# Kernel optimization log

Measured on AMD Instinct MI355X. Metric: run time of the kernel, lower is better.

The kernel has to match this reference:

```python
import jax, jax.numpy as jnp
import numpy as np

N = 200000
E = 600000
H = 128
NUM_EDGE_TYPES = 16
LN_EPS = 1e-5


def setup_inputs() -> dict:
    key = jax.random.key(0)
    ks = jax.random.split(key, 10)
    x = jax.random.normal(ks[0], (N, H), dtype=jnp.float32)
    edge_index = jax.random.randint(ks[1], (2, E), 0, N, dtype=jnp.int32)
    edge_types = jax.random.randint(ks[2], (E,), 0, NUM_EDGE_TYPES, dtype=jnp.int32)
    s = 1.0 / np.sqrt(H)
    edge_emb = jax.random.normal(ks[3], (NUM_EDGE_TYPES, H), dtype=jnp.float32)
    W_self = jax.random.uniform(ks[4], (H, H), dtype=jnp.float32, minval=-s, maxval=s)
    b_self = jax.random.uniform(ks[5], (H,), dtype=jnp.float32, minval=-s, maxval=s)
    W_msg = jax.random.uniform(ks[6], (H, H), dtype=jnp.float32, minval=-s, maxval=s)
    b_msg = jax.random.uniform(ks[7], (H,), dtype=jnp.float32, minval=-s, maxval=s)
    gamma = jnp.ones((H,), dtype=jnp.float32)
    beta = jnp.zeros((H,), dtype=jnp.float32)
    return {
        "x": x, "edge_index": edge_index, "edge_types": edge_types,
        "edge_emb": edge_emb, "W_self": W_self, "b_self": b_self,
        "W_msg": W_msg, "b_msg": b_msg, "gamma": gamma, "beta": beta,
    }


def reference(x, edge_index, edge_types, edge_emb, W_self, b_self, W_msg, b_msg, gamma, beta):
    src = edge_index[0]
    dst = edge_index[1]
    # gather source node features + typed edge embedding: [E, H]
    typed_messages = x[src] + edge_emb[edge_types]
    # scatter-add into destination nodes: [N, H]
    aggregated = jnp.zeros_like(x).at[dst].add(typed_messages)
    # linear epilogue (torch Linear: y = x @ W.T + b)
    out = (x @ W_self.T + b_self) + (aggregated @ W_msg.T + b_msg)
    out = jax.nn.relu(out)
    # LayerNorm over last dim
    mu = jnp.mean(out, axis=-1, keepdims=True)
    var = jnp.mean(jnp.square(out - mu), axis=-1, keepdims=True)
    out = (out - mu) * jax.lax.rsqrt(var + LN_EPS) * gamma + beta
    # dropout is identity in eval mode
    return out
```

## Files before the change

### kernel.cpp

```cpp
#include <hip/hip_runtime.h>
#include <stdint.h>

#define H 128
#define TM 16
#define MAXDEG 24
#define BSTRIDE 32

typedef __attribute__((ext_vector_type(8))) short short8;
typedef __attribute__((ext_vector_type(4))) float f32x4;
typedef __attribute__((ext_vector_type(4))) int i32x4;

__device__ __forceinline__ unsigned short f2bf(float f) {
    union { float f; unsigned u; } v; v.f = f;
    unsigned u = v.u;
    u += 0x7fffu + ((u >> 16) & 1u);
    return (unsigned short)(u >> 16);
}

__device__ __forceinline__ float bf2f(unsigned short u) {
    union { unsigned u; float f; } v; v.u = ((unsigned)u) << 16; return v.f;
}

__device__ __forceinline__ short8 cvt8(f32x4 a, f32x4 b) {
    short8 r;
    r[0] = (short)f2bf(a.x); r[1] = (short)f2bf(a.y);
    r[2] = (short)f2bf(a.z); r[3] = (short)f2bf(a.w);
    r[4] = (short)f2bf(b.x); r[5] = (short)f2bf(b.y);
    r[6] = (short)f2bf(b.z); r[7] = (short)f2bf(b.w);
    return r;
}

__global__ __launch_bounds__(256) void prep_kernel(
    const float* __restrict__ x, const float* __restrict__ emb,
    unsigned short* __restrict__ xb, unsigned short* __restrict__ embb,
    const int* __restrict__ ei, const int* __restrict__ et,
    int* __restrict__ bucket,
    int total8x, int total8e, int E)
{
    int i = blockIdx.x * 256 + threadIdx.x;
    if (i < total8x) {
        f32x4 a = ((const f32x4*)x)[2 * i];
        f32x4 b = ((const f32x4*)x)[2 * i + 1];
        ((short8*)xb)[i] = cvt8(a, b);
    } else if (i < total8x + total8e) {
        int j = i - total8x;
        f32x4 a = ((const f32x4*)emb)[2 * j];
        f32x4 b = ((const f32x4*)emb)[2 * j + 1];
        ((short8*)embb)[j] = cvt8(a, b);
    }
    if (i < E) {
        int src = ei[i];
        int dst = ei[E + i];
        int t   = et[i];
        int* row = bucket + (size_t)dst * BSTRIDE;
        int pos = atomicAdd(row, 1);
        if (pos < MAXDEG) row[1 + pos] = src | (t << 18);
    }
}

__global__ __launch_bounds__(256) void prep_edges_kernel(
    const int* __restrict__ ei, const int* __restrict__ et,
    int* __restrict__ cnt, int* __restrict__ bucket, int E)
{
    int e = blockIdx.x * 256 + threadIdx.x;
    if (e >= E) return;
    int src = ei[e];
    int dst = ei[E + e];
    int t   = et[e];
    int pos = atomicAdd(&cnt[dst], 1);
    if (pos < MAXDEG) bucket[(size_t)dst * MAXDEG + pos] = src | (t << 18);
}

__global__ __launch_bounds__(256) void aggregate_bf16_kernel(
    const unsigned short* __restrict__ xb, const unsigned short* __restrict__ embb,
    const int* __restrict__ bucket,
    const int* __restrict__ ei, const int* __restrict__ et,
    unsigned short* __restrict__ aggb, int N, int E, int T)
{
    __shared__ __align__(16) short emb_s[16 * 136];

    const int tid = threadIdx.x;
    const int l   = tid & 15;
    if (tid < T * 16) {
        int t = tid >> 4;
        *(short8*)&emb_s[t * 136 + l * 8] = *(const short8*)(embb + t * H + l * 8);
    }
    __syncthreads();

    const int nGroups = N >> 4;
    for (int g = blockIdx.x; g < nGroups; g += gridDim.x) {
        const int node = (g << 4) + (tid >> 4);

        const int* row = bucket + (size_t)node * BSTRIDE;
        i32x4 q = *(const i32x4*)row;
        const int c = q.x;

        float acc[8] = {0.f, 0.f, 0.f, 0.f, 0.f, 0.f, 0.f, 0.f};

        if (c <= MAXDEG) {
            {
                const bool b0 = c > 0, b1 = c > 1, b2 = c > 2;
                short8 xv0, xv1, xv2, ev0, ev1, ev2;
                if (b0) {
                    int s = q.y & 0x3FFFF, t = q.y >> 18;
                    xv0 = *(const short8*)(xb + (size_t)s * H + l * 8);
                    ev0 = *(const short8*)&emb_s[t * 136 + l * 8];
                }
                if (b1) {
                    int s = q.z & 0x3FFFF, t = q.z >> 18;
                    xv1 = *(const short8*)(xb + (size_t)s * H + l * 8);
                    ev1 = *(const short8*)&emb_s[t * 136 + l * 8];
                }
                if (b2) {
                    int s = q.w & 0x3FFFF, t = q.w >> 18;
                    xv2 = *(const short8*)(xb + (size_t)s * H + l * 8);
                    ev2 = *(const short8*)&emb_s[t * 136 + l * 8];
                }
                if (b0) {
#pragma unroll
                    for (int j = 0; j < 8; ++j) acc[j] += bf2f((unsigned short)xv0[j]) + bf2f((unsigned short)ev0[j]);
                }
                if (b1) {
#pragma unroll
                    for (int j = 0; j < 8; ++j) acc[j] += bf2f((unsigned short)xv1[j]) + bf2f((unsigned short)ev1[j]);
                }
                if (b2) {
#pragma unroll
                    for (int j = 0; j < 8; ++j) acc[j] += bf2f((unsigned short)xv2[j]) + bf2f((unsigned short)ev2[j]);
                }
            }
            for (int i0 = 3; i0 < c; i0 += 4) {
                i32x4 p = *(const i32x4*)(row + 1 + i0);
                const int rem = c - i0;
                const bool h1 = rem > 1, h2 = rem > 2, h3 = rem > 3;
                short8 xv0, xv1, xv2, xv3, ev0, ev1, ev2, ev3;
                {
                    int s = p.x & 0x3FFFF, t = p.x >> 18;
                    xv0 = *(const short8*)(xb + (size_t)s * H + l * 8);
                    ev0 = *(const short8*)&emb_s[t * 136 + l * 8];
                }
                if (h1) {
                    int s = p.y & 0x3FFFF, t = p.y >> 18;
                    xv1 = *(const short8*)(xb + (size_t)s * H + l * 8);
                    ev1 = *(const short8*)&emb_s[t * 136 + l * 8];
                }
                if (h2) {
                    int s = p.z & 0x3FFFF, t = p.z >> 18;
                    xv2 = *(const short8*)(xb + (size_t)s * H + l * 8);
                    ev2 = *(const short8*)&emb_s[t * 136 + l * 8];
                }
                if (h3) {
                    int s = p.w & 0x3FFFF, t = p.w >> 18;
                    xv3 = *(const short8*)(xb + (size_t)s * H + l * 8);
                    ev3 = *(const short8*)&emb_s[t * 136 + l * 8];
                }
#pragma unroll
                for (int j = 0; j < 8; ++j) acc[j] += bf2f((unsigned short)xv0[j]) + bf2f((unsigned short)ev0[j]);
                if (h1) {
#pragma unroll
                    for (int j = 0; j < 8; ++j) acc[j] += bf2f((unsigned short)xv1[j]) + bf2f((unsigned short)ev1[j]);
                }
                if (h2) {
#pragma unroll
                    for (int j = 0; j < 8; ++j) acc[j] += bf2f((unsigned short)xv2[j]) + bf2f((unsigned short)ev2[j]);
                }
                if (h3) {
#pragma unroll
                    for (int j = 0; j < 8; ++j) acc[j] += bf2f((unsigned short)xv3[j]) + bf2f((unsigned short)ev3[j]);
                }
            }
        } else {
            for (int e = 0; e < E; ++e) {
                if (ei[E + e] == node) {
                    int s = ei[e], t = et[e];
                    short8 xv = *(const short8*)(xb + (size_t)s * H + l * 8);
                    short8 ev = *(const short8*)&emb_s[t * 136 + l * 8];
#pragma unroll
                    for (int j = 0; j < 8; ++j) acc[j] += bf2f((unsigned short)xv[j]) + bf2f((unsigned short)ev[j]);
                }
            }
        }

        short8 r;
#pragma unroll
        for (int j = 0; j < 8; ++j) r[j] = (short)f2bf(acc[j]);
        *(short8*)(aggb + (size_t)node * H + l * 8) = r;
    }
}

__global__ __launch_bounds__(256) void gemm_ln32_kernel(
    const unsigned short* __restrict__ xb, const unsigned short* __restrict__ aggb,
    const float* __restrict__ Wself, const float* __restrict__ bself,
    const float* __restrict__ Wmsg, const float* __restrict__ bmsg,
    const float* __restrict__ gamma, const float* __restrict__ beta,
    float* __restrict__ out, int nSuper)
{
    __shared__ __align__(16) short a_stage[32 * 264];
    __shared__ __align__(16) float o_stage[32 * 132];

    const int tid  = threadIdx.x;
    const int wave = tid >> 6;
    const int lane = tid & 63;
    const int col  = lane & 15;
    const int quad = lane >> 4;

    short8 bfrag[2][8];
    float bias[2];
#pragma unroll
    for (int s = 0; s < 2; ++s) {
        const int h = (wave * 2 + s) * 16 + col;
        bias[s] = bself[h] + bmsg[h];
#pragma unroll
        for (int kst = 0; kst < 8; ++kst) {
            const float* W = (kst < 4) ? Wself : Wmsg;
            const int k0 = (kst & 3) * 32 + quad * 8;
            const float* p = W + (size_t)h * H + k0;
            bfrag[s][kst] = cvt8(*(const f32x4*)p, *(const f32x4*)(p + 4));
        }
    }

    const int lrow = tid >> 4;
    const int l4 = (tid & 15) * 4;
    f32x4 g0  = *(const f32x4*)(gamma + l4);
    f32x4 g1  = *(const f32x4*)(gamma + 64 + l4);
    f32x4 be0 = *(const f32x4*)(beta + l4);
    f32x4 be1 = *(const f32x4*)(beta + 64 + l4);

    const int srow = tid >> 3;
    const int sq   = tid & 7;

    for (int st = blockIdx.x; st < nSuper; st += gridDim.x) {
        const size_t rowBase = (size_t)st * 32;

        {
            const unsigned short* src = (sq < 4)
                ? (xb   + (rowBase + srow) * H + sq * 32)
                : (aggb + (rowBase + srow) * H + (sq - 4) * 32);
            short* dstl = &a_stage[srow * 264 + (sq & 3) * 32 + ((sq >> 2) << 7)];
            *(short8*)(dstl)      = ((const short8*)src)[0];
            *(short8*)(dstl + 8)  = ((const short8*)src)[1];
            *(short8*)(dstl + 16) = ((const short8*)src)[2];
            *(short8*)(dstl + 24) = ((const short8*)src)[3];
        }
        __syncthreads();

        f32x4 acc00 = {0.f,0.f,0.f,0.f}, acc01 = {0.f,0.f,0.f,0.f};
        f32x4 acc10 = {0.f,0.f,0.f,0.f}, acc11 = {0.f,0.f,0.f,0.f};
        {
            short8 afr[8];
#pragma unroll
            for (int kst = 0; kst < 8; ++kst)
                afr[kst] = *(const short8*)&a_stage[col * 264 + kst * 32 + quad * 8];
#pragma unroll
            for (int kst = 0; kst < 8; ++kst) {
                acc00 = __builtin_amdgcn_mfma_f32_16x16x32_bf16(afr[kst], bfrag[0][kst], acc00, 0, 0, 0);
                acc01 = __builtin_amdgcn_mfma_f32_16x16x32_bf16(afr[kst], bfrag[1][kst], acc01, 0, 0, 0);
            }
#pragma unroll
            for (int kst = 0; kst < 8; ++kst)
                afr[kst] = *(const short8*)&a_stage[(16 + col) * 264 + kst * 32 + quad * 8];
#pragma unroll
            for (int kst = 0; kst < 8; ++kst) {
                acc10 = __builtin_amdgcn_mfma_f32_16x16x32_bf16(afr[kst], bfrag[0][kst], acc10, 0, 0, 0);
                acc11 = __builtin_amdgcn_mfma_f32_16x16x32_bf16(afr[kst], bfrag[1][kst], acc11, 0, 0, 0);
            }
        }

        {
            const int h0 = (wave * 2) * 16 + col;
            const int h1 = h0 + 16;
#pragma unroll
            for (int r = 0; r < 4; ++r) {
                const int m = quad * 4 + r;
                float v;
                v = acc00[r] + bias[0]; o_stage[m * 132 + h0]        = v > 0.f ? v : 0.f;
                v = acc01[r] + bias[1]; o_stage[m * 132 + h1]        = v > 0.f ? v : 0.f;
                v = acc10[r] + bias[0]; o_stage[(16 + m) * 132 + h0] = v > 0.f ? v : 0.f;
                v = acc11[r] + bias[1]; o_stage[(16 + m) * 132 + h1] = v > 0.f ? v : 0.f;
            }
        }
        __syncthreads();

#pragma unroll
        for (int half = 0; half < 2; ++half) {
            const int row = half * 16 + lrow;
            const float* orow = &o_stage[row * 132];
            f32x4 va = *(const f32x4*)(orow + l4);
            f32x4 vb = *(const f32x4*)(orow + 64 + l4);

            float s1 = (va.x + va.y + va.z + va.w) + (vb.x + vb.y + vb.z + vb.w);
            float s2 = va.x*va.x + va.y*va.y + va.z*va.z + va.w*va.w
                     + vb.x*vb.x + vb.y*vb.y + vb.z*vb.z + vb.w*vb.w;
#pragma unroll
            for (int m = 1; m < 16; m <<= 1) {
                s1 += __shfl_xor(s1, m, 64);
                s2 += __shfl_xor(s2, m, 64);
            }
            const float mu = s1 * (1.f / 128.f);
            const float var = s2 * (1.f / 128.f) - mu * mu;
            const float rstd = rsqrtf(var + 1e-5f);

            f32x4 o0, o1;
            o0.x = (va.x - mu) * rstd * g0.x + be0.x;
            o0.y = (va.y - mu) * rstd * g0.y + be0.y;
            o0.z = (va.z - mu) * rstd * g0.z + be0.z;
            o0.w = (va.w - mu) * rstd * g0.w + be0.w;
            o1.x = (vb.x - mu) * rstd * g1.x + be1.x;
            o1.y = (vb.y - mu) * rstd * g1.y + be1.y;
            o1.z = (vb.z - mu) * rstd * g1.z + be1.z;
            o1.w = (vb.w - mu) * rstd * g1.w + be1.w;

            float* dst = out + (rowBase + row) * H;
            __builtin_nontemporal_store(o0, (f32x4*)(dst + l4));
            __builtin_nontemporal_store(o1, (f32x4*)(dst + 64 + l4));
        }
    }
}

__global__ __launch_bounds__(256) void aggregate_f32_kernel(
    const float* __restrict__ x, const float* __restrict__ emb,
    const int* __restrict__ cnt, const int* __restrict__ bucket,
    const int* __restrict__ ei, const int* __restrict__ et,
    unsigned short* __restrict__ aggb, int N, int E, int T)
{
    __shared__ __align__(16) float emb_s[16 * 132];

    const int tid = threadIdx.x;
    for (int i = tid; i < T * H; i += 256)
        emb_s[(i >> 7) * 132 + (i & 127)] = emb[i];
    __syncthreads();

    const int l = tid & 15;
    const int nGroups = N >> 4;

    for (int g = blockIdx.x; g < nGroups; g += gridDim.x) {
        const int node = (g << 4) + (tid >> 4);
        const int* b = bucket + (size_t)node * MAXDEG;
        i32x4 p = *(const i32x4*)b;
        const int c = cnt[node];

        f32x4 acc0 = {0.f,0.f,0.f,0.f};
        f32x4 acc1 = {0.f,0.f,0.f,0.f};

        if (c <= MAXDEG) {
            for (int i0 = 0; i0 < c; i0 += 4) {
                if (i0 > 0) p = *(const i32x4*)(b + i0);
                const int rem = c - i0;
                const bool h1 = rem > 1, h2 = rem > 2, h3 = rem > 3;
                f32x4 x00,x01,e00,e01,x10,x11,e10,e11,x20,x21,e20,e21,x30,x31,e30,e31;
                {
                    int s = p.x & 0x3FFFF, t = p.x >> 18;
                    const float* xp = x + (size_t)s * H + l * 8;
                    const float* ep = emb_s + t * 132 + l * 8;
                    x00 = *(const f32x4*)xp; x01 = *(const f32x4*)(xp + 4);
                    e00 = *(const f32x4*)ep; e01 = *(const f32x4*)(ep + 4);
                }
                if (h1) {
                    int s = p.y & 0x3FFFF, t = p.y >> 18;
                    const float* xp = x + (size_t)s * H + l * 8;
                    const float* ep = emb_s + t * 132 + l * 8;
                    x10 = *(const f32x4*)xp; x11 = *(const f32x4*)(xp + 4);
                    e10 = *(const f32x4*)ep; e11 = *(const f32x4*)(ep + 4);
                }
                if (h2) {
                    int s = p.z & 0x3FFFF, t = p.z >> 18;
                    const float* xp = x + (size_t)s * H + l * 8;
                    const float* ep = emb_s + t * 132 + l * 8;
                    x20 = *(const f32x4*)xp; x21 = *(const f32x4*)(xp + 4);
                    e20 = *(const f32x4*)ep; e21 = *(const f32x4*)(ep + 4);
                }
                if (h3) {
                    int s = p.w & 0x3FFFF, t = p.w >> 18;
                    const float* xp = x + (size_t)s * H + l * 8;
                    const float* ep = emb_s + t * 132 + l * 8;
                    x30 = *(const f32x4*)xp; x31 = *(const f32x4*)(xp + 4);
                    e30 = *(const f32x4*)ep; e31 = *(const f32x4*)(ep + 4);
                }
                acc0 += x00 + e00;  acc1 += x01 + e01;
                if (h1) { acc0 += x10 + e10;  acc1 += x11 + e11; }
                if (h2) { acc0 += x20 + e20;  acc1 += x21 + e21; }
                if (h3) { acc0 += x30 + e30;  acc1 += x31 + e31; }
            }
        } else {
            for (int e = 0; e < E; ++e) {
                if (ei[E + e] == node) {
                    int s = ei[e], t = et[e];
                    const float* xp = x + (size_t)s * H + l * 8;
                    const float* ep = emb_s + t * 132 + l * 8;
                    f32x4 a0 = *(const f32x4*)xp, a1 = *(const f32x4*)(xp + 4);
                    f32x4 b0 = *(const f32x4*)ep, b1 = *(const f32x4*)(ep + 4);
                    acc0 += a0 + b0;  acc1 += a1 + b1;
                }
            }
        }
        *(short8*)(aggb + (size_t)node * H + l * 8) = cvt8(acc0, acc1);
    }
}

__global__ __launch_bounds__(256) void gemm_ln16_kernel(
    const float* __restrict__ x, const unsigned short* __restrict__ aggb,
    const float* __restrict__ Wself, const float* __restrict__ bself,
    const float* __restrict__ Wmsg, const float* __restrict__ bmsg,
    const float* __restrict__ gamma, const float* __restrict__ beta,
    float* __restrict__ out, int nTiles)
{
    __shared__ __align__(16) short a_stage[TM * 264];
    __shared__ __align__(16) float o_stage[TM * 132];

    const int tid  = threadIdx.x;
    const int wave = tid >> 6;
    const int lane = tid & 63;
    const int col  = lane & 15;
    const int quad = lane >> 4;

    short8 bfrag[2][8];
    float bias[2];
#pragma unroll
    for (int s = 0; s < 2; ++s) {
        const int h = (wave * 2 + s) * 16 + col;
        bias[s] = bself[h] + bmsg[h];
#pragma unroll
        for (int kst = 0; kst < 8; ++kst) {
            const float* W = (kst < 4) ? Wself : Wmsg;
            const int k0 = (kst & 3) * 32 + quad * 8;
            const float* p = W + (size_t)h * H + k0;
            bfrag[s][kst] = cvt8(*(const f32x4*)p, *(const f32x4*)(p + 4));
        }
    }

    const int lnode = tid >> 4;
    const int f0 = (tid & 15) * 8;
    f32x4 g0  = *(const f32x4*)(gamma + f0);
    f32x4 g1  = *(const f32x4*)(gamma + f0 + 4);
    f32x4 be0 = *(const f32x4*)(beta + f0);
    f32x4 be1 = *(const f32x4*)(beta + f0 + 4);

    const int node = tid >> 4;
    const int seg  = tid & 15;

    for (int tile = blockIdx.x; tile < nTiles; tile += gridDim.x) {
        const size_t rowBase = (size_t)tile * TM;
        if (seg < 8) {
            const float* src = x + (rowBase + node) * H + seg * 16;
            f32x4 v0 = ((const f32x4*)src)[0];
            f32x4 v1 = ((const f32x4*)src)[1];
            f32x4 v2 = ((const f32x4*)src)[2];
            f32x4 v3 = ((const f32x4*)src)[3];
            *(short8*)&a_stage[node * 264 + seg * 16]     = cvt8(v0, v1);
            *(short8*)&a_stage[node * 264 + seg * 16 + 8] = cvt8(v2, v3);
        } else {
            const unsigned short* src = aggb + (rowBase + node) * H + (seg - 8) * 16;
            *(short8*)&a_stage[node * 264 + 128 + (seg - 8) * 16]     = *(const short8*)src;
            *(short8*)&a_stage[node * 264 + 128 + (seg - 8) * 16 + 8] = *(const short8*)(src + 8);
        }
        __syncthreads();

        short8 afr[8];
#pragma unroll
        for (int kst = 0; kst < 8; ++kst)
            afr[kst] = *(const short8*)(&a_stage[col * 264 + kst * 32 + quad * 8]);

        f32x4 acc0 = {0.f,0.f,0.f,0.f};
        f32x4 acc1 = {0.f,0.f,0.f,0.f};
#pragma unroll
        for (int kst = 0; kst < 8; ++kst) {
            acc0 = __builtin_amdgcn_mfma_f32_16x16x32_bf16(afr[kst], bfrag[0][kst], acc0, 0, 0, 0);
            acc1 = __builtin_amdgcn_mfma_f32_16x16x32_bf16(afr[kst], bfrag[1][kst], acc1, 0, 0, 0);
        }

#pragma unroll
        for (int s = 0; s < 2; ++s) {
            const int h = (wave * 2 + s) * 16 + col;
            f32x4 a = s ? acc1 : acc0;
#pragma unroll
            for (int r = 0; r < 4; ++r) {
                const int m = quad * 4 + r;
                float v = a[r] + bias[s];
                o_stage[m * 132 + h] = v > 0.f ? v : 0.f;
            }
        }
        __syncthreads();

        float v[8];
        float s1 = 0.f, s2 = 0.f;
#pragma unroll
        for (int j = 0; j < 8; ++j) {
            v[j] = o_stage[lnode * 132 + f0 + j];
            s1 += v[j];
            s2 += v[j] * v[j];
        }
#pragma unroll
        for (int m = 1; m < 16; m <<= 1) {
            s1 += __shfl_xor(s1, m, 64);
            s2 += __shfl_xor(s2, m, 64);
        }
        const float mu = s1 * (1.f / 128.f);
        const float var = s2 * (1.f / 128.f) - mu * mu;
        const float rstd = rsqrtf(var + 1e-5f);

        f32x4 o0, o1;
        o0.x = (v[0] - mu) * rstd * g0.x + be0.x;
        o0.y = (v[1] - mu) * rstd * g0.y + be0.y;
        o0.z = (v[2] - mu) * rstd * g0.z + be0.z;
        o0.w = (v[3] - mu) * rstd * g0.w + be0.w;
        o1.x = (v[4] - mu) * rstd * g1.x + be1.x;
        o1.y = (v[5] - mu) * rstd * g1.y + be1.y;
        o1.z = (v[6] - mu) * rstd * g1.z + be1.z;
        o1.w = (v[7] - mu) * rstd * g1.w + be1.w;

        float* dst = out + (rowBase + lnode) * H + f0;
        __builtin_nontemporal_store(o0, (f32x4*)dst);
        __builtin_nontemporal_store(o1, (f32x4*)(dst + 4));
    }
}

__global__ __launch_bounds__(256) void scatter_kernel(
    const float* __restrict__ x, const int* __restrict__ ei,
    const int* __restrict__ et, const float* __restrict__ emb,
    float* __restrict__ agg, int E)
{
    int g = blockIdx.x * 256 + threadIdx.x;
    int e = g >> 5;
    int l = g & 31;
    if (e >= E) return;
    int src = ei[e];
    int dst = ei[E + e];
    int t   = et[e];
    f32x4 xv = *(const f32x4*)(x   + (size_t)src * H + l * 4);
    f32x4 ev = *(const f32x4*)(emb + (size_t)t   * H + l * 4);
    float* b = agg + (size_t)dst * H + l * 4;
    atomicAdd(b + 0, xv.x + ev.x);
    atomicAdd(b + 1, xv.y + ev.y);
    atomicAdd(b + 2, xv.z + ev.z);
    atomicAdd(b + 3, xv.w + ev.w);
}

__global__ __launch_bounds__(256) void gemm_ln_f32_kernel(
    const float* __restrict__ x,
    const float* __restrict__ Wself, const float* __restrict__ bself,
    const float* __restrict__ Wmsg, const float* __restrict__ bmsg,
    const float* __restrict__ gamma, const float* __restrict__ beta,
    float* __restrict__ out, int nTiles)
{
    __shared__ __align__(16) short a_stage[TM * 264];
    __shared__ __align__(16) float o_stage[TM * 132];

    const int tid  = threadIdx.x;
    const int wave = tid >> 6;
    const int lane = tid & 63;
    const int col  = lane & 15;
    const int quad = lane >> 4;

    short8 bfrag[2][8];
    float bias[2];
#pragma unroll
    for (int s = 0; s < 2; ++s) {
        const int h = (wave * 2 + s) * 16 + col;
        bias[s] = bself[h] + bmsg[h];
#pragma unroll
        for (int kst = 0; kst < 8; ++kst) {
            const float* W = (kst < 4) ? Wself : Wmsg;
            const int k0 = (kst & 3) * 32 + quad * 8;
            const float* p = W + (size_t)h * H + k0;
            bfrag[s][kst] = cvt8(*(const f32x4*)p, *(const f32x4*)(p + 4));
        }
    }

    const int lnode = tid >> 4;
    const int f0 = (tid & 15) * 8;
    f32x4 g0  = *(const f32x4*)(gamma + f0);
    f32x4 g1  = *(const f32x4*)(gamma + f0 + 4);
    f32x4 be0 = *(const f32x4*)(beta + f0);
    f32x4 be1 = *(const f32x4*)(beta + f0 + 4);

    for (int tile = blockIdx.x; tile < nTiles; tile += gridDim.x) {
        const size_t rowBase = (size_t)tile * TM;
        {
            const int node = tid >> 4;
            const int seg  = tid & 15;
            const int k0   = seg * 16;
            const float* src = (seg < 8)
                ? (x   + (rowBase + node) * H + k0)
                : (out + (rowBase + node) * H + (k0 - 128));
            f32x4 v0 = ((const f32x4*)src)[0];
            f32x4 v1 = ((const f32x4*)src)[1];
            f32x4 v2 = ((const f32x4*)src)[2];
            f32x4 v3 = ((const f32x4*)src)[3];
            *(short8*)(&a_stage[node * 264 + k0])     = cvt8(v0, v1);
            *(short8*)(&a_stage[node * 264 + k0 + 8]) = cvt8(v2, v3);
        }
        __syncthreads();

        short8 afr[8];
#pragma unroll
        for (int kst = 0; kst < 8; ++kst)
            afr[kst] = *(const short8*)(&a_stage[col * 264 + kst * 32 + quad * 8]);

        f32x4 acc0 = {0.f,0.f,0.f,0.f};
        f32x4 acc1 = {0.f,0.f,0.f,0.f};
#pragma unroll
        for (int kst = 0; kst < 8; ++kst) {
            acc0 = __builtin_amdgcn_mfma_f32_16x16x32_bf16(afr[kst], bfrag[0][kst], acc0, 0, 0, 0);
            acc1 = __builtin_amdgcn_mfma_f32_16x16x32_bf16(afr[kst], bfrag[1][kst], acc1, 0, 0, 0);
        }

#pragma unroll
        for (int s = 0; s < 2; ++s) {
            const int h = (wave * 2 + s) * 16 + col;
            f32x4 a = s ? acc1 : acc0;
#pragma unroll
            for (int r = 0; r < 4; ++r) {
                const int m = quad * 4 + r;
                float v = a[r] + bias[s];
                o_stage[m * 132 + h] = v > 0.f ? v : 0.f;
            }
        }
        __syncthreads();

        float v[8];
        float s1 = 0.f, s2 = 0.f;
#pragma unroll
        for (int j = 0; j < 8; ++j) {
            v[j] = o_stage[lnode * 132 + f0 + j];
            s1 += v[j];
            s2 += v[j] * v[j];
        }
#pragma unroll
        for (int m = 1; m < 16; m <<= 1) {
            s1 += __shfl_xor(s1, m, 64);
            s2 += __shfl_xor(s2, m, 64);
        }
        const float mu = s1 * (1.f / 128.f);
        const float var = s2 * (1.f / 128.f) - mu * mu;
        const float rstd = rsqrtf(var + 1e-5f);

        f32x4 o0, o1;
        o0.x = (v[0] - mu) * rstd * g0.x + be0.x;
        o0.y = (v[1] - mu) * rstd * g0.y + be0.y;
        o0.z = (v[2] - mu) * rstd * g0.z + be0.z;
        o0.w = (v[3] - mu) * rstd * g0.w + be0.w;
        o1.x = (v[4] - mu) * rstd * g1.x + be1.x;
        o1.y = (v[5] - mu) * rstd * g1.y + be1.y;
        o1.z = (v[6] - mu) * rstd * g1.z + be1.z;
        o1.w = (v[7] - mu) * rstd * g1.w + be1.w;

        float* dst = out + (rowBase + lnode) * H + f0;
        *(f32x4*)(dst)     = o0;
        *(f32x4*)(dst + 4) = o1;
    }
}

extern "C" void kernel_launch(void* const* d_in, const int* in_sizes, int n_in,
                              void* d_out, int out_size, void* d_ws, size_t ws_size,
                              hipStream_t stream) {
    const float* x     = (const float*)d_in[0];
    const int*   ei    = (const int*)d_in[1];
    const int*   et    = (const int*)d_in[2];
    const float* emb   = (const float*)d_in[3];
    const float* Wself = (const float*)d_in[4];
    const float* bself = (const float*)d_in[5];
    const float* Wmsg  = (const float*)d_in[6];
    const float* bmsg  = (const float*)d_in[7];
    const float* gamma = (const float*)d_in[8];
    const float* beta  = (const float*)d_in[9];
    float* out = (float*)d_out;

    const int E = in_sizes[2];
    const int N = in_sizes[0] / H;
    const int T = in_sizes[3] / H;
    const int nTiles = N / TM;

    auto rnd = [](size_t b) { return (b + 255) & ~(size_t)255; };
    const size_t sz_xb   = rnd((size_t)N * H * 2);
    const size_t sz_embb = rnd((size_t)T * H * 2);
    const size_t sz_agg  = rnd((size_t)N * H * 2);
    const size_t sz_bkt32 = rnd((size_t)N * BSTRIDE * 4);
    const size_t sz_cnt  = rnd((size_t)N * 4);
    const size_t sz_bkt24 = rnd((size_t)N * MAXDEG * 4);
    const size_t needA = sz_xb + sz_embb + sz_agg + sz_bkt32;
    const size_t needB = sz_agg + sz_cnt + sz_bkt24;

    const bool okT = (T <= 16) && (N <= (1 << 18));
    const bool tierA = okT && (ws_size >= needA) && (N % 32 == 0);
    const bool tierB = okT && (ws_size >= needB) && (N % TM == 0);

    if (tierA) {
        uint8_t* p = (uint8_t*)d_ws;
        unsigned short* xb   = (unsigned short*)p;  p += sz_xb;
        unsigned short* embb = (unsigned short*)p;  p += sz_embb;
        unsigned short* aggb = (unsigned short*)p;  p += sz_agg;
        int* bucket = (int*)p;

        hipMemsetAsync(bucket, 0, (size_t)N * BSTRIDE * sizeof(int), stream);

        const int t8x = N * H / 8, t8e = T * H / 8;
        int prepWork = (t8x + t8e) > E ? (t8x + t8e) : E;
        prep_kernel<<<(prepWork + 255) / 256, 256, 0, stream>>>(
            x, emb, xb, embb, ei, et, bucket, t8x, t8e, E);

        const int nGroups = N >> 4;
        int aggGrid = nGroups < 6250 ? nGroups : 6250;
        aggregate_bf16_kernel<<<aggGrid, 256, 0, stream>>>(
            xb, embb, bucket, ei, et, aggb, N, E, T);

        const int nSuper = N / 32;
        int gemmGrid = nSuper < 3125 ? nSuper : 3125;
        gemm_ln32_kernel<<<gemmGrid, 256, 0, stream>>>(
            xb, aggb, Wself, bself, Wmsg, bmsg, gamma, beta, out, nSuper);
    } else if (tierB) {
        uint8_t* p = (uint8_t*)d_ws;
        unsigned short* aggb = (unsigned short*)p;  p += sz_agg;
        int* cnt    = (int*)p;                      p += sz_cnt;
        int* bucket = (int*)p;

        hipMemsetAsync(cnt, 0, (size_t)N * sizeof(int), stream);

        if (E > 0) {
            prep_edges_kernel<<<(E + 255) / 256, 256, 0, stream>>>(
                ei, et, cnt, bucket, E);
        }
        const int nGroups = N >> 4;
        int aggGrid = nGroups < 4096 ? nGroups : 4096;
        aggregate_f32_kernel<<<aggGrid, 256, 0, stream>>>(
            x, emb, cnt, bucket, ei, et, aggb, N, E, T);

        int gemmGrid = nTiles < 2048 ? nTiles : 2048;
        gemm_ln16_kernel<<<gemmGrid, 256, 0, stream>>>(
            x, aggb, Wself, bself, Wmsg, bmsg, gamma, beta, out, nTiles);
    } else {
        hipMemsetAsync(out, 0, (size_t)N * H * sizeof(float), stream);
        const long long sthreads = (long long)E * 32;
        scatter_kernel<<<(int)((sthreads + 255) / 256), 256, 0, stream>>>(
            x, ei, et, emb, out, E);
        int grid = 2500;
        if (grid > nTiles) grid = nTiles;
        gemm_ln_f32_kernel<<<grid, 256, 0, stream>>>(
            x, Wself, bself, Wmsg, bmsg, gamma, beta, out, nTiles);
    }
}
```

Measured before the change: 316.0 us.

## Shrink edge buckets to 16 ints with global overflow list, alias GEMM smem

Edge buckets per node shrink from 32 to 16 ints, holding 15 entries inline. Extra edges spill into a small global overflow list that high-degree nodes scan, with the full edge scan kept as a fallback. This halves the bucket memset and read traffic. The prep kernel now handles 4 conversions per thread with nontemporal loads and splits the edge work across blocks. The GEMM kernel shares one LDS buffer between the A stage and the output stage, adding barriers, and the grid cap rises to 8192. The risk is that nodes with degree above 15 scan the whole overflow list serially.

```diff
diff --git a/kernel.cpp b/kernel.cpp
--- a/kernel.cpp
+++ b/kernel.cpp
@@ -5,6 +5,8 @@
 #define TM 16
 #define MAXDEG 24
 #define BSTRIDE 32
+#define BSTR16 16
+#define OVFCAP 4096
 
 typedef __attribute__((ext_vector_type(8))) short short8;
 typedef __attribute__((ext_vector_type(4))) float f32x4;
@@ -30,31 +32,54 @@
     return r;
 }
 
+__device__ __forceinline__ void gadd(int entry, const unsigned short* xb,
+                                     const short* emb_s, int l, float* acc) {
+    int s = entry & 0x3FFFF, t = entry >> 18;
+    short8 xv = *(const short8*)(xb + (size_t)s * H + l * 8);
+    short8 ev = *(const short8*)&emb_s[t * 136 + l * 8];
+#pragma unroll
+    for (int j = 0; j < 8; ++j)
+        acc[j] += bf2f((unsigned short)xv[j]) + bf2f((unsigned short)ev[j]);
+}
+
 __global__ __launch_bounds__(256) void prep_kernel(
     const float* __restrict__ x, const float* __restrict__ emb,
     unsigned short* __restrict__ xb, unsigned short* __restrict__ embb,
     const int* __restrict__ ei, const int* __restrict__ et,
-    int* __restrict__ bucket,
-    int total8x, int total8e, int E)
+    int* __restrict__ bucket, int* __restrict__ ovf,
+    int total8x, int total8, int E, int eb)
 {
-    int i = blockIdx.x * 256 + threadIdx.x;
-    if (i < total8x) {
-        f32x4 a = ((const f32x4*)x)[2 * i];
-        f32x4 b = ((const f32x4*)x)[2 * i + 1];
-        ((short8*)xb)[i] = cvt8(a, b);
-    } else if (i < total8x + total8e) {
-        int j = i - total8x;
-        f32x4 a = ((const f32x4*)emb)[2 * j];
-        f32x4 b = ((const f32x4*)emb)[2 * j + 1];
-        ((short8*)embb)[j] = cvt8(a, b);
-    }
-    if (i < E) {
-        int src = ei[i];
-        int dst = ei[E + i];
-        int t   = et[i];
-        int* row = bucket + (size_t)dst * BSTRIDE;
+    const int tid = threadIdx.x;
+    const int base = blockIdx.x << 10;
+#pragma unroll
+    for (int k = 0; k < 4; ++k) {
+        int idx = base + (k << 8) + tid;
+        if (idx < total8x) {
+            f32x4 a = __builtin_nontemporal_load(((const f32x4*)x) + 2 * idx);
+            f32x4 b = __builtin_nontemporal_load(((const f32x4*)x) + 2 * idx + 1);
+            ((short8*)xb)[idx] = cvt8(a, b);
+        } else if (idx < total8) {
+            int j = idx - total8x;
+            f32x4 a = __builtin_nontemporal_load(((const f32x4*)emb) + 2 * j);
+            f32x4 b = __builtin_nontemporal_load(((const f32x4*)emb) + 2 * j + 1);
+            ((short8*)embb)[j] = cvt8(a, b);
+        }
+    }
+    int e0 = blockIdx.x * eb;
+    int e1 = e0 + eb; if (e1 > E) e1 = E;
+    for (int e = e0 + tid; e < e1; e += 256) {
+        int src = ei[e];
+        int dst = ei[E + e];
+        int t   = et[e];
+        int entry = src | (t << 18);
+        int* row = bucket + ((size_t)dst << 4);
         int pos = atomicAdd(row, 1);
-        if (pos < MAXDEG) row[1 + pos] = src | (t << 18);
+        if (pos < 15) {
+            row[1 + pos] = entry;
+        } else {
+            int j = atomicAdd(ovf, 1);
+            if (j < OVFCAP) { ovf[8 + 2 * j] = dst; ovf[8 + 2 * j + 1] = entry; }
+        }
     }
 }
 
@@ -73,7 +98,7 @@
 
 __global__ __launch_bounds__(256) void aggregate_bf16_kernel(
     const unsigned short* __restrict__ xb, const unsigned short* __restrict__ embb,
-    const int* __restrict__ bucket,
+    const int* __restrict__ bucket, const int* __restrict__ ovf,
     const int* __restrict__ ei, const int* __restrict__ et,
     unsigned short* __restrict__ aggb, int N, int E, int T)
 {
@@ -91,15 +116,23 @@
     for (int g = blockIdx.x; g < nGroups; g += gridDim.x) {
         const int node = (g << 4) + (tid >> 4);
 
-        const int* row = bucket + (size_t)node * BSTRIDE;
+        const int* row = bucket + ((size_t)node << 4);
         i32x4 q = *(const i32x4*)row;
         const int c = q.x;
 
         float acc[8] = {0.f, 0.f, 0.f, 0.f, 0.f, 0.f, 0.f, 0.f};
 
-        if (c <= MAXDEG) {
+        bool fullscan = false;
+        int cc = c, nov = 0;
+        if (c > 15) {
+            nov = ovf[0];
+            if (nov > OVFCAP) fullscan = true;
+            cc = 15;
+        }
+
+        if (!fullscan) {
             {
-                const bool b0 = c > 0, b1 = c > 1, b2 = c > 2;
+                const bool b0 = cc > 0, b1 = cc > 1, b2 = cc > 2;
                 short8 xv0, xv1, xv2, ev0, ev1, ev2;
                 if (b0) {
                     int s = q.y & 0x3FFFF, t = q.y >> 18;
@@ -129,9 +162,9 @@
                     for (int j = 0; j < 8; ++j) acc[j] += bf2f((unsigned short)xv2[j]) + bf2f((unsigned short)ev2[j]);
                 }
             }
-            for (int i0 = 3; i0 < c; i0 += 4) {
+            for (int i0 = 3; i0 < cc; i0 += 4) {
                 i32x4 p = *(const i32x4*)(row + 1 + i0);
-                const int rem = c - i0;
+                const int rem = cc - i0;
                 const bool h1 = rem > 1, h2 = rem > 2, h3 = rem > 3;
                 short8 xv0, xv1, xv2, xv3, ev0, ev1, ev2, ev3;
                 {
@@ -169,15 +202,14 @@
                     for (int j = 0; j < 8; ++j) acc[j] += bf2f((unsigned short)xv3[j]) + bf2f((unsigned short)ev3[j]);
                 }
             }
+            if (c > 15) {
+                for (int j = 0; j < nov; ++j) {
+                    if (ovf[8 + 2 * j] == node) gadd(ovf[8 + 2 * j + 1], xb, emb_s, l, acc);
+                }
+            }
         } else {
             for (int e = 0; e < E; ++e) {
-                if (ei[E + e] == node) {
-                    int s = ei[e], t = et[e];
-                    short8 xv = *(const short8*)(xb + (size_t)s * H + l * 8);
-                    short8 ev = *(const short8*)&emb_s[t * 136 + l * 8];
-#pragma unroll
-                    for (int j = 0; j < 8; ++j) acc[j] += bf2f((unsigned short)xv[j]) + bf2f((unsigned short)ev[j]);
-                }
+                if (ei[E + e] == node) gadd(ei[e] | (et[e] << 18), xb, emb_s, l, acc);
             }
         }
 
@@ -195,8 +227,9 @@
     const float* __restrict__ gamma, const float* __restrict__ beta,
     float* __restrict__ out, int nSuper)
 {
-    __shared__ __align__(16) short a_stage[32 * 264];
-    __shared__ __align__(16) float o_stage[32 * 132];
+    __shared__ __align__(16) char smem_u[32 * 264 * 2];
+    short* a_stage = (short*)smem_u;
+    float* o_stage = (float*)smem_u;
 
     const int tid  = threadIdx.x;
     const int wave = tid >> 6;
@@ -231,6 +264,7 @@
 
     for (int st = blockIdx.x; st < nSuper; st += gridDim.x) {
         const size_t rowBase = (size_t)st * 32;
+        __syncthreads();
 
         {
             const unsigned short* src = (sq < 4)
@@ -265,6 +299,7 @@
                 acc11 = __builtin_amdgcn_mfma_f32_16x16x32_bf16(afr[kst], bfrag[1][kst], acc11, 0, 0, 0);
             }
         }
+        __syncthreads();
 
         {
             const int h0 = (wave * 2) * 16 + col;
@@ -671,13 +706,14 @@
     const int nTiles = N / TM;
 
     auto rnd = [](size_t b) { return (b + 255) & ~(size_t)255; };
-    const size_t sz_xb   = rnd((size_t)N * H * 2);
-    const size_t sz_embb = rnd((size_t)T * H * 2);
-    const size_t sz_agg  = rnd((size_t)N * H * 2);
-    const size_t sz_bkt32 = rnd((size_t)N * BSTRIDE * 4);
-    const size_t sz_cnt  = rnd((size_t)N * 4);
+    const size_t sz_xb    = rnd((size_t)N * H * 2);
+    const size_t sz_embb  = rnd((size_t)T * H * 2);
+    const size_t sz_agg   = rnd((size_t)N * H * 2);
+    const size_t sz_bkt16 = rnd((size_t)N * BSTR16 * 4);
+    const size_t sz_ovf   = rnd((size_t)(8 + 2 * OVFCAP) * 4);
+    const size_t sz_cnt   = rnd((size_t)N * 4);
     const size_t sz_bkt24 = rnd((size_t)N * MAXDEG * 4);
-    const size_t needA = sz_xb + sz_embb + sz_agg + sz_bkt32;
+    const size_t needA = sz_xb + sz_embb + sz_agg + sz_bkt16 + sz_ovf;
     const size_t needB = sz_agg + sz_cnt + sz_bkt24;
 
     const bool okT = (T <= 16) && (N <= (1 << 18));
@@ -689,22 +725,25 @@
         unsigned short* xb   = (unsigned short*)p;  p += sz_xb;
         unsigned short* embb = (unsigned short*)p;  p += sz_embb;
         unsigned short* aggb = (unsigned short*)p;  p += sz_agg;
-        int* bucket = (int*)p;
-
-        hipMemsetAsync(bucket, 0, (size_t)N * BSTRIDE * sizeof(int), stream);
+        int* bucket = (int*)p;                      p += sz_bkt16;
+        int* ovf    = (int*)p;
+
+        hipMemsetAsync(bucket, 0, sz_bkt16 + sz_ovf, stream);
 
         const int t8x = N * H / 8, t8e = T * H / 8;
-        int prepWork = (t8x + t8e) > E ? (t8x + t8e) : E;
-        prep_kernel<<<(prepWork + 255) / 256, 256, 0, stream>>>(
-            x, emb, xb, embb, ei, et, bucket, t8x, t8e, E);
+        const int total8 = t8x + t8e;
+        const int nConv = (total8 + 1023) >> 10;
+        const int eb = (E + nConv - 1) / nConv;
+        prep_kernel<<<nConv, 256, 0, stream>>>(
+            x, emb, xb, embb, ei, et, bucket, ovf, t8x, total8, E, eb);
 
         const int nGroups = N >> 4;
         int aggGrid = nGroups < 6250 ? nGroups : 6250;
         aggregate_bf16_kernel<<<aggGrid, 256, 0, stream>>>(
-            xb, embb, bucket, ei, et, aggb, N, E, T);
+            xb, embb, bucket, ovf, ei, et, aggb, N, E, T);
 
         const int nSuper = N / 32;
-        int gemmGrid = nSuper < 3125 ? nSuper : 3125;
+        int gemmGrid = nSuper < 8192 ? nSuper : 8192;
         gemm_ln32_kernel<<<gemmGrid, 256, 0, stream>>>(
             xb, aggb, Wself, bself, Wmsg, bmsg, gamma, beta, out, nSuper);
     } else if (tierB) {
```

After: 353.8 us. 12.0% more time.
